# Optimization experiments

Hardware: AMD Instinct MI355X
Metric: run time of the kernel (lower is better)

## Reference

```python
import jax, jax.numpy as jnp
import numpy as np

N_NODES = 50000
N_EDGES = 800000
NFEAT = 96
NHID = 128
EPS = 1e-12  # F.normalize default eps


def setup_inputs() -> dict:
    key = jax.random.key(0)
    k1, k2, k3, k4 = jax.random.split(key, 4)
    edge_index = jax.random.randint(k1, (2, N_EDGES), 0, N_NODES, dtype=jnp.int64)
    x = jax.random.normal(k2, (N_NODES, NFEAT), dtype=jnp.float32)
    # Glorot-ish scaling for linear weights
    W_l = jax.random.normal(k3, (NHID, NFEAT), dtype=jnp.float32) * (1.0 / np.sqrt(NFEAT))
    b_l = jnp.zeros((NHID,), dtype=jnp.float32)
    W_r = jax.random.normal(k4, (NHID, NFEAT), dtype=jnp.float32) * (1.0 / np.sqrt(NFEAT))
    return {"edge_index": edge_index, "x": x, "W_l": W_l, "b_l": b_l, "W_r": W_r}


def reference(edge_index, x, W_l, b_l, W_r):
    # PyG SAGEConv, aggr='mean', root_weight=True, normalize=True
    src, dst = edge_index[0], edge_index[1]
    # gather source features, scatter-sum into destination nodes
    msg_sum = jax.ops.segment_sum(x[src], dst, num_segments=N_NODES)  # [N, nfeat]
    deg = jax.ops.segment_sum(jnp.ones((edge_index.shape[1],), dtype=x.dtype),
                              dst, num_segments=N_NODES)
    agg = msg_sum / jnp.maximum(deg, 1.0)[:, None]  # mean; isolated nodes -> 0
    out = agg @ W_l.T + b_l + x @ W_r.T  # [N, nhid]
    # L2 normalize per node (F.normalize p=2, dim=-1)
    norm = jnp.linalg.norm(out, axis=-1, keepdims=True)
    return out / jnp.maximum(norm, EPS)
```

## Files before the change

### kernel.cpp

```cpp
#include <hip/hip_runtime.h>


typedef __attribute__((ext_vector_type(8))) short short8;
typedef __attribute__((ext_vector_type(4))) float floatx4;

constexpr int kNodes = 50000;
constexpr int kEdges = 800000;
constexpr int kF = 96;
constexpr int kH = 128;
constexpr int kEllW = 32;
constexpr int kSpillCap = 4096;
constexpr int kBktRange = kNodes / 8;

constexpr size_t kXhOff    = 0;
constexpr size_t kWhOff    = 19200000;
constexpr size_t kEllOff   = 19249152;
constexpr size_t kCurOff   = 22449152;
constexpr size_t kSpcOff   = 22649152;
constexpr size_t kSpillOff = 22649168;

constexpr int kPeriods    = 782;
constexpr int kMegaBlocks = kPeriods * 11;
constexpr int kPrepBlocks = kPeriods * 3;
constexpr int kPrepItems  = kNodes * kF / 8 + kH * 192 / 8;
constexpr int kPrepStride = kPrepBlocks * 256;

constexpr int kRowS = 104;

__device__ __forceinline__ unsigned pack2_bf16(float a, float b) {
  unsigned ua = __float_as_uint(a), ub = __float_as_uint(b);
  ua = (ua + 0x7fffu + ((ua >> 16) & 1u)) >> 16;
  ub = (ub + 0x7fffu + ((ub >> 16) & 1u)) >> 16;
  return ua | (ub << 16);
}
__device__ __forceinline__ float bf_lo(unsigned u) { return __uint_as_float(u << 16); }
__device__ __forceinline__ float bf_hi(unsigned u) { return __uint_as_float(u & 0xffff0000u); }

__device__ __forceinline__ void ell_insert(int dst, int src, int* cursor,
                                           ushort* ell, unsigned* spill,
                                           int* spillCnt) {
  const int slot = atomicAdd(&cursor[dst], 1);
  if (slot < kEllW) {
    ell[(size_t)dst * kEllW + ((slot & 3) << 3) + (slot >> 2)] = (ushort)src;
  } else {
    const int sp = atomicAdd(spillCnt, 1);
    if (sp < kSpillCap) spill[sp] = ((unsigned)dst << 16) | (unsigned)src;
  }
}

__global__ void __launch_bounds__(256)
mega_kernel(const int* __restrict__ ei, const float* __restrict__ x,
            const float* __restrict__ Wl, const float* __restrict__ Wr,
            uint4* __restrict__ xh4, uint4* __restrict__ wh4,
            int* __restrict__ cursor, ushort* __restrict__ ell,
            unsigned* __restrict__ spill, int* __restrict__ spillCnt) {
  const int p = blockIdx.x / 11;
  const int r = blockIdx.x % 11;
  if (r < 8) {
    const int g = blockIdx.x & 7;
    const int lo = g * kBktRange, hi = lo + kBktRange;
    const int base = p * 1024 + threadIdx.x;
    int d[4];
#pragma unroll
    for (int k = 0; k < 4; ++k) {
      const int e = base + k * 256;
      d[k] = (e < kEdges) ? ei[kEdges + e] : -1;
    }
#pragma unroll
    for (int k = 0; k < 4; ++k) {
      if (d[k] >= lo && d[k] < hi) {
        const int e = base + k * 256;
        ell_insert(d[k], ei[e], cursor, ell, spill, spillCnt);
      }
    }
    return;
  }
  constexpr int kCvt = kNodes * kF / 8;
  const int pid = p * 3 + (r - 8);
  for (int i = pid * 256 + threadIdx.x; i < kPrepItems; i += kPrepStride) {
    if (i < kCvt) {
      const float4 v0 = reinterpret_cast<const float4*>(x)[i * 2];
      const float4 v1 = reinterpret_cast<const float4*>(x)[i * 2 + 1];
      uint4 o;
      o.x = pack2_bf16(v0.x, v0.y);
      o.y = pack2_bf16(v0.z, v0.w);
      o.z = pack2_bf16(v1.x, v1.y);
      o.w = pack2_bf16(v1.z, v1.w);
      xh4[i] = o;
    } else {
      const int j = i - kCvt;
      const int row = j / 24, chunk = j % 24;
      const float* src = (chunk < 12) ? (Wl + (size_t)row * kF + chunk * 8)
                                      : (Wr + (size_t)row * kF + (chunk - 12) * 8);
      const float4 v0 = reinterpret_cast<const float4*>(src)[0];
      const float4 v1 = reinterpret_cast<const float4*>(src)[1];
      uint4 o;
      o.x = pack2_bf16(v0.x, v0.y);
      o.y = pack2_bf16(v0.z, v0.w);
      o.z = pack2_bf16(v1.x, v1.y);
      o.w = pack2_bf16(v1.z, v1.w);
      wh4[j] = o;
    }
  }
}

__global__ void __launch_bounds__(256)
gm_kernel(const uint4* __restrict__ xh4, const int* __restrict__ cursor,
          const ushort* __restrict__ ell, const unsigned* __restrict__ spill,
          const int* __restrict__ spillCnt, const uint4* __restrict__ wh4,
          const float* __restrict__ bl, float* __restrict__ out) {
  __shared__ __align__(16) short sAgg[16 * kRowS];
  __shared__ float sP[4][4][4];

  const int wave = threadIdx.x >> 6, lane = threadIdx.x & 63;
  const int g = blockIdx.x & 7;
  const int j = blockIdx.x >> 3;
  const int tstart = (g * 3125) >> 3;
  const int tend = ((g + 1) * 3125) >> 3;
  const int tile = tstart + j;
  if (tile >= tend) return;
  const int base = tile * 16;

  const int slot = lane / 12;
  const int c = lane % 12;
  const bool gactive = lane < 48;
  const int slotc = gactive ? slot : 0;
  const int sc = min(*spillCnt, kSpillCap);

#pragma unroll
  for (int it = 0; it < 2; ++it) {
    const int nA = base + wave * 4 + it * 2;
    const int nB = nA + 1;
    const int degA = cursor[nA];
    const int degB = cursor[nB];
    const int dmA = min(degA, kEllW);
    const int dmB = min(degB, kEllW);

    const uint4 ivA = *reinterpret_cast<const uint4*>(
        ell + (size_t)nA * kEllW + (slotc << 3));
    const uint4 ivB = *reinterpret_cast<const uint4*>(
        ell + (size_t)nB * kEllW + (slotc << 3));
    const unsigned wa[4] = {ivA.x, ivA.y, ivA.z, ivA.w};
    const unsigned wb[4] = {ivB.x, ivB.y, ivB.z, ivB.w};

    float a0 = 0.f, a1 = 0.f, a2 = 0.f, a3 = 0.f,
          a4 = 0.f, a5 = 0.f, a6 = 0.f, a7 = 0.f;
    float b0 = 0.f, b1 = 0.f, b2 = 0.f, b3 = 0.f,
          b4 = 0.f, b5 = 0.f, b6 = 0.f, b7 = 0.f;

#pragma unroll
    for (int k = 0; k < 8; ++k) {
      const int idx = (k << 2) + slot;
      const int srcA = (k & 1) ? (int)(wa[k >> 1] >> 16) : (int)(wa[k >> 1] & 0xffffu);
      const int srcB = (k & 1) ? (int)(wb[k >> 1] >> 16) : (int)(wb[k >> 1] & 0xffffu);
      if (gactive && idx < dmA) {
        const uint4 v = xh4[(size_t)srcA * 12 + c];
        a0 += bf_lo(v.x); a1 += bf_hi(v.x);
        a2 += bf_lo(v.y); a3 += bf_hi(v.y);
        a4 += bf_lo(v.z); a5 += bf_hi(v.z);
        a6 += bf_lo(v.w); a7 += bf_hi(v.w);
      }
      if (gactive && idx < dmB) {
        const uint4 v = xh4[(size_t)srcB * 12 + c];
        b0 += bf_lo(v.x); b1 += bf_hi(v.x);
        b2 += bf_lo(v.y); b3 += bf_hi(v.y);
        b4 += bf_lo(v.z); b5 += bf_hi(v.z);
        b6 += bf_lo(v.w); b7 += bf_hi(v.w);
      }
    }
    for (int jj = 0; jj < sc; ++jj) {
      const unsigned pr = spill[jj];
      const int pd = (int)(pr >> 16);
      if (lane < 12 && (pd == nA || pd == nB)) {
        const uint4 v = xh4[(size_t)(pr & 0xffffu) * 12 + c];
        if (pd == nA) {
          a0 += bf_lo(v.x); a1 += bf_hi(v.x);
          a2 += bf_lo(v.y); a3 += bf_hi(v.y);
          a4 += bf_lo(v.z); a5 += bf_hi(v.z);
          a6 += bf_lo(v.w); a7 += bf_hi(v.w);
        } else {
          b0 += bf_lo(v.x); b1 += bf_hi(v.x);
          b2 += bf_lo(v.y); b3 += bf_hi(v.y);
          b4 += bf_lo(v.z); b5 += bf_hi(v.z);
          b6 += bf_lo(v.w); b7 += bf_hi(v.w);
        }
      }
    }
    a0 += __shfl(a0, lane + 24, 64); a1 += __shfl(a1, lane + 24, 64);
    a2 += __shfl(a2, lane + 24, 64); a3 += __shfl(a3, lane + 24, 64);
    a4 += __shfl(a4, lane + 24, 64); a5 += __shfl(a5, lane + 24, 64);
    a6 += __shfl(a6, lane + 24, 64); a7 += __shfl(a7, lane + 24, 64);
    a0 += __shfl(a0, lane + 12, 64); a1 += __shfl(a1, lane + 12, 64);
    a2 += __shfl(a2, lane + 12, 64); a3 += __shfl(a3, lane + 12, 64);
    a4 += __shfl(a4, lane + 12, 64); a5 += __shfl(a5, lane + 12, 64);
    a6 += __shfl(a6, lane + 12, 64); a7 += __shfl(a7, lane + 12, 64);
    b0 += __shfl(b0, lane + 24, 64); b1 += __shfl(b1, lane + 24, 64);
    b2 += __shfl(b2, lane + 24, 64); b3 += __shfl(b3, lane + 24, 64);
    b4 += __shfl(b4, lane + 24, 64); b5 += __shfl(b5, lane + 24, 64);
    b6 += __shfl(b6, lane + 24, 64); b7 += __shfl(b7, lane + 24, 64);
    b0 += __shfl(b0, lane + 12, 64); b1 += __shfl(b1, lane + 12, 64);
    b2 += __shfl(b2, lane + 12, 64); b3 += __shfl(b3, lane + 12, 64);
    b4 += __shfl(b4, lane + 12, 64); b5 += __shfl(b5, lane + 12, 64);
    b6 += __shfl(b6, lane + 12, 64); b7 += __shfl(b7, lane + 12, 64);

    if (lane < 12) {
      const float invA = 1.0f / fmaxf((float)degA, 1.0f);
      uint4 o;
      o.x = pack2_bf16(a0 * invA, a1 * invA);
      o.y = pack2_bf16(a2 * invA, a3 * invA);
      o.z = pack2_bf16(a4 * invA, a5 * invA);
      o.w = pack2_bf16(a6 * invA, a7 * invA);
      *reinterpret_cast<uint4*>(&sAgg[(wave * 4 + it * 2) * kRowS + c * 8]) = o;
      const float invB = 1.0f / fmaxf((float)degB, 1.0f);
      uint4 p;
      p.x = pack2_bf16(b0 * invB, b1 * invB);
      p.y = pack2_bf16(b2 * invB, b3 * invB);
      p.z = pack2_bf16(b4 * invB, b5 * invB);
      p.w = pack2_bf16(b6 * invB, b7 * invB);
      *reinterpret_cast<uint4*>(&sAgg[(wave * 4 + it * 2 + 1) * kRowS + c * 8]) = p;
    }
  }
  __syncthreads();

  const int r = lane & 15, q = lane >> 4;
  const int cg0 = wave * 2;
  const short8* xhS = reinterpret_cast<const short8*>(xh4);
  const short8* whS = reinterpret_cast<const short8*>(wh4);

  floatx4 acc[2] = {};
#pragma unroll
  for (int ks = 0; ks < 6; ++ks) {
    short8 a;
    if (ks < 3) {
      a = *reinterpret_cast<const short8*>(&sAgg[r * kRowS + (ks * 4 + q) * 8]);
    } else {
      a = xhS[(size_t)(base + r) * 12 + (ks - 3) * 4 + q];
    }
#pragma unroll
    for (int i = 0; i < 2; ++i) {
      const short8 b = whS[((cg0 + i) * 16 + r) * 24 + ks * 4 + q];
      acc[i] = __builtin_amdgcn_mfma_f32_16x16x32_bf16(a, b, acc[i], 0, 0, 0);
    }
  }

  float p0 = 0.f, p1 = 0.f, p2 = 0.f, p3 = 0.f;
#pragma unroll
  for (int i = 0; i < 2; ++i) {
    const float bb = bl[(cg0 + i) * 16 + r];
    acc[i][0] += bb; acc[i][1] += bb; acc[i][2] += bb; acc[i][3] += bb;
    p0 += acc[i][0] * acc[i][0];
    p1 += acc[i][1] * acc[i][1];
    p2 += acc[i][2] * acc[i][2];
    p3 += acc[i][3] * acc[i][3];
  }
#pragma unroll
  for (int off = 1; off < 16; off <<= 1) {
    p0 += __shfl_xor(p0, off, 64);
    p1 += __shfl_xor(p1, off, 64);
    p2 += __shfl_xor(p2, off, 64);
    p3 += __shfl_xor(p3, off, 64);
  }
  if (r == 0) {
    sP[wave][q][0] = p0; sP[wave][q][1] = p1;
    sP[wave][q][2] = p2; sP[wave][q][3] = p3;
  }
  __syncthreads();
  const float t0 = sP[0][q][0] + sP[1][q][0] + sP[2][q][0] + sP[3][q][0];
  const float t1 = sP[0][q][1] + sP[1][q][1] + sP[2][q][1] + sP[3][q][1];
  const float t2 = sP[0][q][2] + sP[1][q][2] + sP[2][q][2] + sP[3][q][2];
  const float t3 = sP[0][q][3] + sP[1][q][3] + sP[2][q][3] + sP[3][q][3];
  const float s0 = 1.0f / fmaxf(sqrtf(t0), 1e-12f);
  const float s1 = 1.0f / fmaxf(sqrtf(t1), 1e-12f);
  const float s2 = 1.0f / fmaxf(sqrtf(t2), 1e-12f);
  const float s3 = 1.0f / fmaxf(sqrtf(t3), 1e-12f);

#pragma unroll
  for (int i = 0; i < 2; ++i) {
    const int col = (cg0 + i) * 16 + r;
    float* o = out + (size_t)(base + q * 4) * kH + col;
    o[0 * kH] = acc[i][0] * s0;
    o[1 * kH] = acc[i][1] * s1;
    o[2 * kH] = acc[i][2] * s2;
    o[3 * kH] = acc[i][3] * s3;
  }
}

extern "C" void kernel_launch(void* const* d_in, const int* in_sizes, int n_in,
                              void* d_out, int out_size, void* d_ws, size_t ws_size,
                              hipStream_t stream) {
  const int*   ei = (const int*)d_in[0];
  const float* x  = (const float*)d_in[1];
  const float* Wl = (const float*)d_in[2];
  const float* bl = (const float*)d_in[3];
  const float* Wr = (const float*)d_in[4];
  float* out = (float*)d_out;

  char* ws = (char*)d_ws;
  uint4*    xh4      = (uint4*)(ws + kXhOff);
  uint4*    wh4      = (uint4*)(ws + kWhOff);
  ushort*   ell      = (ushort*)(ws + kEllOff);
  int*      cursor   = (int*)(ws + kCurOff);
  int*      spillCnt = (int*)(ws + kSpcOff);
  unsigned* spill    = (unsigned*)(ws + kSpillOff);

  hipMemsetAsync(ws + kCurOff, 0, 200008, stream);

  mega_kernel<<<kMegaBlocks, 256, 0, stream>>>(ei, x, Wl, Wr, xh4, wh4, cursor,
                                               ell, spill, spillCnt);

  gm_kernel<<<391 * 8, 256, 0, stream>>>(xh4, cursor, ell, spill, spillCnt,
                                         wh4, bl, out);
}
```

Baseline: 101.0 us.

## Pad degree counters to cache-line stride and gather four nodes per pass

Degree/cursor counters are spread to one per 64-byte line to reduce atomic contention among neighbouring destination nodes during ELL construction. The aggregation step now loads ELL indices and degrees for four nodes up front and interleaves their gathers in a single loop, increasing outstanding memory requests. In exchange, the counter memset grows sixteenfold, degree reads become strided, and register pressure rises.

```diff
diff --git a/kernel.cpp b/kernel.cpp
--- a/kernel.cpp
+++ b/kernel.cpp
@@ -11,13 +11,14 @@
 constexpr int kEllW = 32;
 constexpr int kSpillCap = 4096;
 constexpr int kBktRange = kNodes / 8;
+constexpr int kCurStride = 16;
 
 constexpr size_t kXhOff    = 0;
 constexpr size_t kWhOff    = 19200000;
 constexpr size_t kEllOff   = 19249152;
 constexpr size_t kCurOff   = 22449152;
-constexpr size_t kSpcOff   = 22649152;
-constexpr size_t kSpillOff = 22649168;
+constexpr size_t kSpcOff   = 25649152;
+constexpr size_t kSpillOff = 25649168;
 
 constexpr int kPeriods    = 782;
 constexpr int kMegaBlocks = kPeriods * 11;
@@ -39,7 +40,7 @@
 __device__ __forceinline__ void ell_insert(int dst, int src, int* cursor,
                                            ushort* ell, unsigned* spill,
                                            int* spillCnt) {
-  const int slot = atomicAdd(&cursor[dst], 1);
+  const int slot = atomicAdd(&cursor[(size_t)dst * kCurStride], 1);
   if (slot < kEllW) {
     ell[(size_t)dst * kEllW + ((slot & 3) << 3) + (slot >> 2)] = (ushort)src;
   } else {
@@ -126,98 +127,77 @@
   const bool gactive = lane < 48;
   const int slotc = gactive ? slot : 0;
   const int sc = min(*spillCnt, kSpillCap);
-
-#pragma unroll
-  for (int it = 0; it < 2; ++it) {
-    const int nA = base + wave * 4 + it * 2;
-    const int nB = nA + 1;
-    const int degA = cursor[nA];
-    const int degB = cursor[nB];
-    const int dmA = min(degA, kEllW);
-    const int dmB = min(degB, kEllW);
-
-    const uint4 ivA = *reinterpret_cast<const uint4*>(
-        ell + (size_t)nA * kEllW + (slotc << 3));
-    const uint4 ivB = *reinterpret_cast<const uint4*>(
-        ell + (size_t)nB * kEllW + (slotc << 3));
-    const unsigned wa[4] = {ivA.x, ivA.y, ivA.z, ivA.w};
-    const unsigned wb[4] = {ivB.x, ivB.y, ivB.z, ivB.w};
-
-    float a0 = 0.f, a1 = 0.f, a2 = 0.f, a3 = 0.f,
-          a4 = 0.f, a5 = 0.f, a6 = 0.f, a7 = 0.f;
-    float b0 = 0.f, b1 = 0.f, b2 = 0.f, b3 = 0.f,
-          b4 = 0.f, b5 = 0.f, b6 = 0.f, b7 = 0.f;
-
-#pragma unroll
-    for (int k = 0; k < 8; ++k) {
-      const int idx = (k << 2) + slot;
-      const int srcA = (k & 1) ? (int)(wa[k >> 1] >> 16) : (int)(wa[k >> 1] & 0xffffu);
-      const int srcB = (k & 1) ? (int)(wb[k >> 1] >> 16) : (int)(wb[k >> 1] & 0xffffu);
-      if (gactive && idx < dmA) {
-        const uint4 v = xh4[(size_t)srcA * 12 + c];
-        a0 += bf_lo(v.x); a1 += bf_hi(v.x);
-        a2 += bf_lo(v.y); a3 += bf_hi(v.y);
-        a4 += bf_lo(v.z); a5 += bf_hi(v.z);
-        a6 += bf_lo(v.w); a7 += bf_hi(v.w);
+  const int n0 = base + wave * 4;
+
+  int deg[4], dm[4];
+  uint4 iv[4];
+#pragma unroll
+  for (int n = 0; n < 4; ++n) {
+    deg[n] = cursor[(size_t)(n0 + n) * kCurStride];
+    iv[n] = *reinterpret_cast<const uint4*>(
+        ell + (size_t)(n0 + n) * kEllW + (slotc << 3));
+  }
+#pragma unroll
+  for (int n = 0; n < 4; ++n) dm[n] = min(deg[n], kEllW);
+
+  float acc[4][8];
+#pragma unroll
+  for (int n = 0; n < 4; ++n)
+#pragma unroll
+    for (int k = 0; k < 8; ++k) acc[n][k] = 0.f;
+
+#pragma unroll
+  for (int k = 0; k < 8; ++k) {
+    const int idx = (k << 2) + slot;
+#pragma unroll
+    for (int n = 0; n < 4; ++n) {
+      const unsigned wrd = (k < 2) ? iv[n].x
+                         : (k < 4) ? iv[n].y
+                         : (k < 6) ? iv[n].z : iv[n].w;
+      const int src = (k & 1) ? (int)(wrd >> 16) : (int)(wrd & 0xffffu);
+      if (gactive && idx < dm[n]) {
+        const uint4 v = xh4[(size_t)src * 12 + c];
+        acc[n][0] += bf_lo(v.x); acc[n][1] += bf_hi(v.x);
+        acc[n][2] += bf_lo(v.y); acc[n][3] += bf_hi(v.y);
+        acc[n][4] += bf_lo(v.z); acc[n][5] += bf_hi(v.z);
+        acc[n][6] += bf_lo(v.w); acc[n][7] += bf_hi(v.w);
       }
-      if (gactive && idx < dmB) {
-        const uint4 v = xh4[(size_t)srcB * 12 + c];
-        b0 += bf_lo(v.x); b1 += bf_hi(v.x);
-        b2 += bf_lo(v.y); b3 += bf_hi(v.y);
-        b4 += bf_lo(v.z); b5 += bf_hi(v.z);
-        b6 += bf_lo(v.w); b7 += bf_hi(v.w);
-      }
-    }
-    for (int jj = 0; jj < sc; ++jj) {
-      const unsigned pr = spill[jj];
-      const int pd = (int)(pr >> 16);
-      if (lane < 12 && (pd == nA || pd == nB)) {
-        const uint4 v = xh4[(size_t)(pr & 0xffffu) * 12 + c];
-        if (pd == nA) {
-          a0 += bf_lo(v.x); a1 += bf_hi(v.x);
-          a2 += bf_lo(v.y); a3 += bf_hi(v.y);
-          a4 += bf_lo(v.z); a5 += bf_hi(v.z);
-          a6 += bf_lo(v.w); a7 += bf_hi(v.w);
-        } else {
-          b0 += bf_lo(v.x); b1 += bf_hi(v.x);
-          b2 += bf_lo(v.y); b3 += bf_hi(v.y);
-          b4 += bf_lo(v.z); b5 += bf_hi(v.z);
-          b6 += bf_lo(v.w); b7 += bf_hi(v.w);
+    }
+  }
+  for (int jj = 0; jj < sc; ++jj) {
+    const unsigned pr = spill[jj];
+    const int rel = (int)(pr >> 16) - n0;
+    if (lane < 12 && rel >= 0 && rel < 4) {
+      const uint4 v = xh4[(size_t)(pr & 0xffffu) * 12 + c];
+#pragma unroll
+      for (int n = 0; n < 4; ++n) {
+        if (rel == n) {
+          acc[n][0] += bf_lo(v.x); acc[n][1] += bf_hi(v.x);
+          acc[n][2] += bf_lo(v.y); acc[n][3] += bf_hi(v.y);
+          acc[n][4] += bf_lo(v.z); acc[n][5] += bf_hi(v.z);
+          acc[n][6] += bf_lo(v.w); acc[n][7] += bf_hi(v.w);
         }
       }
     }
-    a0 += __shfl(a0, lane + 24, 64); a1 += __shfl(a1, lane + 24, 64);
-    a2 += __shfl(a2, lane + 24, 64); a3 += __shfl(a3, lane + 24, 64);
-    a4 += __shfl(a4, lane + 24, 64); a5 += __shfl(a5, lane + 24, 64);
-    a6 += __shfl(a6, lane + 24, 64); a7 += __shfl(a7, lane + 24, 64);
-    a0 += __shfl(a0, lane + 12, 64); a1 += __shfl(a1, lane + 12, 64);
-    a2 += __shfl(a2, lane + 12, 64); a3 += __shfl(a3, lane + 12, 64);
-    a4 += __shfl(a4, lane + 12, 64); a5 += __shfl(a5, lane + 12, 64);
-    a6 += __shfl(a6, lane + 12, 64); a7 += __shfl(a7, lane + 12, 64);
-    b0 += __shfl(b0, lane + 24, 64); b1 += __shfl(b1, lane + 24, 64);
-    b2 += __shfl(b2, lane + 24, 64); b3 += __shfl(b3, lane + 24, 64);
-    b4 += __shfl(b4, lane + 24, 64); b5 += __shfl(b5, lane + 24, 64);
-    b6 += __shfl(b6, lane + 24, 64); b7 += __shfl(b7, lane + 24, 64);
-    b0 += __shfl(b0, lane + 12, 64); b1 += __shfl(b1, lane + 12, 64);
-    b2 += __shfl(b2, lane + 12, 64); b3 += __shfl(b3, lane + 12, 64);
-    b4 += __shfl(b4, lane + 12, 64); b5 += __shfl(b5, lane + 12, 64);
-    b6 += __shfl(b6, lane + 12, 64); b7 += __shfl(b7, lane + 12, 64);
-
-    if (lane < 12) {
-      const float invA = 1.0f / fmaxf((float)degA, 1.0f);
+  }
+#pragma unroll
+  for (int n = 0; n < 4; ++n) {
+#pragma unroll
+    for (int k = 0; k < 8; ++k) {
+      acc[n][k] += __shfl(acc[n][k], lane + 24, 64);
+      acc[n][k] += __shfl(acc[n][k], lane + 12, 64);
+    }
+  }
+  if (lane < 12) {
+#pragma unroll
+    for (int n = 0; n < 4; ++n) {
+      const float inv = 1.0f / fmaxf((float)deg[n], 1.0f);
       uint4 o;
-      o.x = pack2_bf16(a0 * invA, a1 * invA);
-      o.y = pack2_bf16(a2 * invA, a3 * invA);
-      o.z = pack2_bf16(a4 * invA, a5 * invA);
-      o.w = pack2_bf16(a6 * invA, a7 * invA);
-      *reinterpret_cast<uint4*>(&sAgg[(wave * 4 + it * 2) * kRowS + c * 8]) = o;
-      const float invB = 1.0f / fmaxf((float)degB, 1.0f);
-      uint4 p;
-      p.x = pack2_bf16(b0 * invB, b1 * invB);
-      p.y = pack2_bf16(b2 * invB, b3 * invB);
-      p.z = pack2_bf16(b4 * invB, b5 * invB);
-      p.w = pack2_bf16(b6 * invB, b7 * invB);
-      *reinterpret_cast<uint4*>(&sAgg[(wave * 4 + it * 2 + 1) * kRowS + c * 8]) = p;
+      o.x = pack2_bf16(acc[n][0] * inv, acc[n][1] * inv);
+      o.y = pack2_bf16(acc[n][2] * inv, acc[n][3] * inv);
+      o.z = pack2_bf16(acc[n][4] * inv, acc[n][5] * inv);
+      o.w = pack2_bf16(acc[n][6] * inv, acc[n][7] * inv);
+      *reinterpret_cast<uint4*>(&sAgg[(wave * 4 + n) * kRowS + c * 8]) = o;
     }
   }
   __syncthreads();
@@ -227,7 +207,7 @@
   const short8* xhS = reinterpret_cast<const short8*>(xh4);
   const short8* whS = reinterpret_cast<const short8*>(wh4);
 
-  floatx4 acc[2] = {};
+  floatx4 fac[2] = {};
 #pragma unroll
   for (int ks = 0; ks < 6; ++ks) {
     short8 a;
@@ -239,7 +219,7 @@
 #pragma unroll
     for (int i = 0; i < 2; ++i) {
       const short8 b = whS[((cg0 + i) * 16 + r) * 24 + ks * 4 + q];
-      acc[i] = __builtin_amdgcn_mfma_f32_16x16x32_bf16(a, b, acc[i], 0, 0, 0);
+      fac[i] = __builtin_amdgcn_mfma_f32_16x16x32_bf16(a, b, fac[i], 0, 0, 0);
     }
   }
 
@@ -247,11 +227,11 @@
 #pragma unroll
   for (int i = 0; i < 2; ++i) {
     const float bb = bl[(cg0 + i) * 16 + r];
-    acc[i][0] += bb; acc[i][1] += bb; acc[i][2] += bb; acc[i][3] += bb;
-    p0 += acc[i][0] * acc[i][0];
-    p1 += acc[i][1] * acc[i][1];
-    p2 += acc[i][2] * acc[i][2];
-    p3 += acc[i][3] * acc[i][3];
+    fac[i][0] += bb; fac[i][1] += bb; fac[i][2] += bb; fac[i][3] += bb;
+    p0 += fac[i][0] * fac[i][0];
+    p1 += fac[i][1] * fac[i][1];
+    p2 += fac[i][2] * fac[i][2];
+    p3 += fac[i][3] * fac[i][3];
   }
 #pragma unroll
   for (int off = 1; off < 16; off <<= 1) {
@@ -278,10 +258,10 @@
   for (int i = 0; i < 2; ++i) {
     const int col = (cg0 + i) * 16 + r;
     float* o = out + (size_t)(base + q * 4) * kH + col;
-    o[0 * kH] = acc[i][0] * s0;
-    o[1 * kH] = acc[i][1] * s1;
-    o[2 * kH] = acc[i][2] * s2;
-    o[3 * kH] = acc[i][3] * s3;
+    o[0 * kH] = fac[i][0] * s0;
+    o[1 * kH] = fac[i][1] * s1;
+    o[2 * kH] = fac[i][2] * s2;
+    o[3 * kH] = fac[i][3] * s3;
   }
 }
 
@@ -303,7 +283,7 @@
   int*      spillCnt = (int*)(ws + kSpcOff);
   unsigned* spill    = (unsigned*)(ws + kSpillOff);
 
-  hipMemsetAsync(ws + kCurOff, 0, 200008, stream);
+  hipMemsetAsync(ws + kCurOff, 0, 3200008, stream);
 
   mega_kernel<<<kMegaBlocks, 256, 0, stream>>>(ei, x, Wl, Wr, xh4, wh4, cursor,
                                                ell, spill, spillCnt);
```

Measured after the change: 102.4 us. About the same (+1.3%).

## Pad degree cursors to 64B stride and use 8 waves per gather tile

Applied to the files above, without the earlier changes.

Each node's degree counter now sits on its own 64-byte slot, so atomics from different nodes no longer contend on the same cache line. The memset grows from 200 KB to 3.2 MB to clear the padded array. The aggregate-and-project kernel now runs 512 threads per block: each wave gathers neighbours for two nodes instead of four and issues one MFMA output column group instead of two. This adds gather parallelism, but the extra memset traffic and the scattered degree reads are new costs.

```diff
diff --git a/kernel.cpp b/kernel.cpp
--- a/kernel.cpp
+++ b/kernel.cpp
@@ -11,13 +11,14 @@
 constexpr int kEllW = 32;
 constexpr int kSpillCap = 4096;
 constexpr int kBktRange = kNodes / 8;
+constexpr int kCurStride = 16;
 
 constexpr size_t kXhOff    = 0;
 constexpr size_t kWhOff    = 19200000;
 constexpr size_t kEllOff   = 19249152;
 constexpr size_t kCurOff   = 22449152;
-constexpr size_t kSpcOff   = 22649152;
-constexpr size_t kSpillOff = 22649168;
+constexpr size_t kSpcOff   = 25649152;
+constexpr size_t kSpillOff = 25649168;
 
 constexpr int kPeriods    = 782;
 constexpr int kMegaBlocks = kPeriods * 11;
@@ -39,7 +40,7 @@
 __device__ __forceinline__ void ell_insert(int dst, int src, int* cursor,
                                            ushort* ell, unsigned* spill,
                                            int* spillCnt) {
-  const int slot = atomicAdd(&cursor[dst], 1);
+  const int slot = atomicAdd(&cursor[(size_t)dst * kCurStride], 1);
   if (slot < kEllW) {
     ell[(size_t)dst * kEllW + ((slot & 3) << 3) + (slot >> 2)] = (ushort)src;
   } else {
@@ -104,13 +105,13 @@
   }
 }
 
-__global__ void __launch_bounds__(256)
+__global__ void __launch_bounds__(512)
 gm_kernel(const uint4* __restrict__ xh4, const int* __restrict__ cursor,
           const ushort* __restrict__ ell, const unsigned* __restrict__ spill,
           const int* __restrict__ spillCnt, const uint4* __restrict__ wh4,
           const float* __restrict__ bl, float* __restrict__ out) {
   __shared__ __align__(16) short sAgg[16 * kRowS];
-  __shared__ float sP[4][4][4];
+  __shared__ float sP[8][4][4];
 
   const int wave = threadIdx.x >> 6, lane = threadIdx.x & 63;
   const int g = blockIdx.x & 7;
@@ -127,107 +128,104 @@
   const int slotc = gactive ? slot : 0;
   const int sc = min(*spillCnt, kSpillCap);
 
-#pragma unroll
-  for (int it = 0; it < 2; ++it) {
-    const int nA = base + wave * 4 + it * 2;
-    const int nB = nA + 1;
-    const int degA = cursor[nA];
-    const int degB = cursor[nB];
-    const int dmA = min(degA, kEllW);
-    const int dmB = min(degB, kEllW);
-
-    const uint4 ivA = *reinterpret_cast<const uint4*>(
-        ell + (size_t)nA * kEllW + (slotc << 3));
-    const uint4 ivB = *reinterpret_cast<const uint4*>(
-        ell + (size_t)nB * kEllW + (slotc << 3));
-    const unsigned wa[4] = {ivA.x, ivA.y, ivA.z, ivA.w};
-    const unsigned wb[4] = {ivB.x, ivB.y, ivB.z, ivB.w};
-
-    float a0 = 0.f, a1 = 0.f, a2 = 0.f, a3 = 0.f,
-          a4 = 0.f, a5 = 0.f, a6 = 0.f, a7 = 0.f;
-    float b0 = 0.f, b1 = 0.f, b2 = 0.f, b3 = 0.f,
-          b4 = 0.f, b5 = 0.f, b6 = 0.f, b7 = 0.f;
-
-#pragma unroll
-    for (int k = 0; k < 8; ++k) {
-      const int idx = (k << 2) + slot;
-      const int srcA = (k & 1) ? (int)(wa[k >> 1] >> 16) : (int)(wa[k >> 1] & 0xffffu);
-      const int srcB = (k & 1) ? (int)(wb[k >> 1] >> 16) : (int)(wb[k >> 1] & 0xffffu);
-      if (gactive && idx < dmA) {
-        const uint4 v = xh4[(size_t)srcA * 12 + c];
+  const int nA = base + wave * 2;
+  const int nB = nA + 1;
+  const int degA = cursor[(size_t)nA * kCurStride];
+  const int degB = cursor[(size_t)nB * kCurStride];
+  const int dmA = min(degA, kEllW);
+  const int dmB = min(degB, kEllW);
+
+  const uint4 ivA = *reinterpret_cast<const uint4*>(
+      ell + (size_t)nA * kEllW + (slotc << 3));
+  const uint4 ivB = *reinterpret_cast<const uint4*>(
+      ell + (size_t)nB * kEllW + (slotc << 3));
+  const unsigned wa[4] = {ivA.x, ivA.y, ivA.z, ivA.w};
+  const unsigned wb[4] = {ivB.x, ivB.y, ivB.z, ivB.w};
+
+  float a0 = 0.f, a1 = 0.f, a2 = 0.f, a3 = 0.f,
+        a4 = 0.f, a5 = 0.f, a6 = 0.f, a7 = 0.f;
+  float b0 = 0.f, b1 = 0.f, b2 = 0.f, b3 = 0.f,
+        b4 = 0.f, b5 = 0.f, b6 = 0.f, b7 = 0.f;
+
+#pragma unroll
+  for (int k = 0; k < 8; ++k) {
+    const int idx = (k << 2) + slot;
+    const int srcA = (k & 1) ? (int)(wa[k >> 1] >> 16) : (int)(wa[k >> 1] & 0xffffu);
+    const int srcB = (k & 1) ? (int)(wb[k >> 1] >> 16) : (int)(wb[k >> 1] & 0xffffu);
+    if (gactive && idx < dmA) {
+      const uint4 v = xh4[(size_t)srcA * 12 + c];
+      a0 += bf_lo(v.x); a1 += bf_hi(v.x);
+      a2 += bf_lo(v.y); a3 += bf_hi(v.y);
+      a4 += bf_lo(v.z); a5 += bf_hi(v.z);
+      a6 += bf_lo(v.w); a7 += bf_hi(v.w);
+    }
+    if (gactive && idx < dmB) {
+      const uint4 v = xh4[(size_t)srcB * 12 + c];
+      b0 += bf_lo(v.x); b1 += bf_hi(v.x);
+      b2 += bf_lo(v.y); b3 += bf_hi(v.y);
+      b4 += bf_lo(v.z); b5 += bf_hi(v.z);
+      b6 += bf_lo(v.w); b7 += bf_hi(v.w);
+    }
+  }
+  for (int jj = 0; jj < sc; ++jj) {
+    const unsigned pr = spill[jj];
+    const int pd = (int)(pr >> 16);
+    if (lane < 12 && (pd == nA || pd == nB)) {
+      const uint4 v = xh4[(size_t)(pr & 0xffffu) * 12 + c];
+      if (pd == nA) {
         a0 += bf_lo(v.x); a1 += bf_hi(v.x);
         a2 += bf_lo(v.y); a3 += bf_hi(v.y);
         a4 += bf_lo(v.z); a5 += bf_hi(v.z);
         a6 += bf_lo(v.w); a7 += bf_hi(v.w);
-      }
-      if (gactive && idx < dmB) {
-        const uint4 v = xh4[(size_t)srcB * 12 + c];
+      } else {
         b0 += bf_lo(v.x); b1 += bf_hi(v.x);
         b2 += bf_lo(v.y); b3 += bf_hi(v.y);
         b4 += bf_lo(v.z); b5 += bf_hi(v.z);
         b6 += bf_lo(v.w); b7 += bf_hi(v.w);
       }
     }
-    for (int jj = 0; jj < sc; ++jj) {
-      const unsigned pr = spill[jj];
-      const int pd = (int)(pr >> 16);
-      if (lane < 12 && (pd == nA || pd == nB)) {
-        const uint4 v = xh4[(size_t)(pr & 0xffffu) * 12 + c];
-        if (pd == nA) {
-          a0 += bf_lo(v.x); a1 += bf_hi(v.x);
-          a2 += bf_lo(v.y); a3 += bf_hi(v.y);
-          a4 += bf_lo(v.z); a5 += bf_hi(v.z);
-          a6 += bf_lo(v.w); a7 += bf_hi(v.w);
-        } else {
-          b0 += bf_lo(v.x); b1 += bf_hi(v.x);
-          b2 += bf_lo(v.y); b3 += bf_hi(v.y);
-          b4 += bf_lo(v.z); b5 += bf_hi(v.z);
-          b6 += bf_lo(v.w); b7 += bf_hi(v.w);
-        }
-      }
-    }
-    a0 += __shfl(a0, lane + 24, 64); a1 += __shfl(a1, lane + 24, 64);
-    a2 += __shfl(a2, lane + 24, 64); a3 += __shfl(a3, lane + 24, 64);
-    a4 += __shfl(a4, lane + 24, 64); a5 += __shfl(a5, lane + 24, 64);
-    a6 += __shfl(a6, lane + 24, 64); a7 += __shfl(a7, lane + 24, 64);
-    a0 += __shfl(a0, lane + 12, 64); a1 += __shfl(a1, lane + 12, 64);
-    a2 += __shfl(a2, lane + 12, 64); a3 += __shfl(a3, lane + 12, 64);
-    a4 += __shfl(a4, lane + 12, 64); a5 += __shfl(a5, lane + 12, 64);
-    a6 += __shfl(a6, lane + 12, 64); a7 += __shfl(a7, lane + 12, 64);
-    b0 += __shfl(b0, lane + 24, 64); b1 += __shfl(b1, lane + 24, 64);
-    b2 += __shfl(b2, lane + 24, 64); b3 += __shfl(b3, lane + 24, 64);
-    b4 += __shfl(b4, lane + 24, 64); b5 += __shfl(b5, lane + 24, 64);
-    b6 += __shfl(b6, lane + 24, 64); b7 += __shfl(b7, lane + 24, 64);
-    b0 += __shfl(b0, lane + 12, 64); b1 += __shfl(b1, lane + 12, 64);
-    b2 += __shfl(b2, lane + 12, 64); b3 += __shfl(b3, lane + 12, 64);
-    b4 += __shfl(b4, lane + 12, 64); b5 += __shfl(b5, lane + 12, 64);
-    b6 += __shfl(b6, lane + 12, 64); b7 += __shfl(b7, lane + 12, 64);
-
-    if (lane < 12) {
-      const float invA = 1.0f / fmaxf((float)degA, 1.0f);
-      uint4 o;
-      o.x = pack2_bf16(a0 * invA, a1 * invA);
-      o.y = pack2_bf16(a2 * invA, a3 * invA);
-      o.z = pack2_bf16(a4 * invA, a5 * invA);
-      o.w = pack2_bf16(a6 * invA, a7 * invA);
-      *reinterpret_cast<uint4*>(&sAgg[(wave * 4 + it * 2) * kRowS + c * 8]) = o;
-      const float invB = 1.0f / fmaxf((float)degB, 1.0f);
-      uint4 p;
-      p.x = pack2_bf16(b0 * invB, b1 * invB);
-      p.y = pack2_bf16(b2 * invB, b3 * invB);
-      p.z = pack2_bf16(b4 * invB, b5 * invB);
-      p.w = pack2_bf16(b6 * invB, b7 * invB);
-      *reinterpret_cast<uint4*>(&sAgg[(wave * 4 + it * 2 + 1) * kRowS + c * 8]) = p;
-    }
+  }
+  a0 += __shfl(a0, lane + 24, 64); a1 += __shfl(a1, lane + 24, 64);
+  a2 += __shfl(a2, lane + 24, 64); a3 += __shfl(a3, lane + 24, 64);
+  a4 += __shfl(a4, lane + 24, 64); a5 += __shfl(a5, lane + 24, 64);
+  a6 += __shfl(a6, lane + 24, 64); a7 += __shfl(a7, lane + 24, 64);
+  a0 += __shfl(a0, lane + 12, 64); a1 += __shfl(a1, lane + 12, 64);
+  a2 += __shfl(a2, lane + 12, 64); a3 += __shfl(a3, lane + 12, 64);
+  a4 += __shfl(a4, lane + 12, 64); a5 += __shfl(a5, lane + 12, 64);
+  a6 += __shfl(a6, lane + 12, 64); a7 += __shfl(a7, lane + 12, 64);
+  b0 += __shfl(b0, lane + 24, 64); b1 += __shfl(b1, lane + 24, 64);
+  b2 += __shfl(b2, lane + 24, 64); b3 += __shfl(b3, lane + 24, 64);
+  b4 += __shfl(b4, lane + 24, 64); b5 += __shfl(b5, lane + 24, 64);
+  b6 += __shfl(b6, lane + 24, 64); b7 += __shfl(b7, lane + 24, 64);
+  b0 += __shfl(b0, lane + 12, 64); b1 += __shfl(b1, lane + 12, 64);
+  b2 += __shfl(b2, lane + 12, 64); b3 += __shfl(b3, lane + 12, 64);
+  b4 += __shfl(b4, lane + 12, 64); b5 += __shfl(b5, lane + 12, 64);
+  b6 += __shfl(b6, lane + 12, 64); b7 += __shfl(b7, lane + 12, 64);
+
+  if (lane < 12) {
+    const float invA = 1.0f / fmaxf((float)degA, 1.0f);
+    uint4 o;
+    o.x = pack2_bf16(a0 * invA, a1 * invA);
+    o.y = pack2_bf16(a2 * invA, a3 * invA);
+    o.z = pack2_bf16(a4 * invA, a5 * invA);
+    o.w = pack2_bf16(a6 * invA, a7 * invA);
+    *reinterpret_cast<uint4*>(&sAgg[(wave * 2) * kRowS + c * 8]) = o;
+    const float invB = 1.0f / fmaxf((float)degB, 1.0f);
+    uint4 p;
+    p.x = pack2_bf16(b0 * invB, b1 * invB);
+    p.y = pack2_bf16(b2 * invB, b3 * invB);
+    p.z = pack2_bf16(b4 * invB, b5 * invB);
+    p.w = pack2_bf16(b6 * invB, b7 * invB);
+    *reinterpret_cast<uint4*>(&sAgg[(wave * 2 + 1) * kRowS + c * 8]) = p;
   }
   __syncthreads();
 
   const int r = lane & 15, q = lane >> 4;
-  const int cg0 = wave * 2;
+  const int cg = wave;
   const short8* xhS = reinterpret_cast<const short8*>(xh4);
   const short8* whS = reinterpret_cast<const short8*>(wh4);
 
-  floatx4 acc[2] = {};
+  floatx4 fac = {};
 #pragma unroll
   for (int ks = 0; ks < 6; ++ks) {
     short8 a;
@@ -236,23 +234,16 @@
     } else {
       a = xhS[(size_t)(base + r) * 12 + (ks - 3) * 4 + q];
     }
-#pragma unroll
-    for (int i = 0; i < 2; ++i) {
-      const short8 b = whS[((cg0 + i) * 16 + r) * 24 + ks * 4 + q];
-      acc[i] = __builtin_amdgcn_mfma_f32_16x16x32_bf16(a, b, acc[i], 0, 0, 0);
-    }
-  }
-
-  float p0 = 0.f, p1 = 0.f, p2 = 0.f, p3 = 0.f;
-#pragma unroll
-  for (int i = 0; i < 2; ++i) {
-    const float bb = bl[(cg0 + i) * 16 + r];
-    acc[i][0] += bb; acc[i][1] += bb; acc[i][2] += bb; acc[i][3] += bb;
-    p0 += acc[i][0] * acc[i][0];
-    p1 += acc[i][1] * acc[i][1];
-    p2 += acc[i][2] * acc[i][2];
-    p3 += acc[i][3] * acc[i][3];
-  }
+    const short8 b = whS[(cg * 16 + r) * 24 + ks * 4 + q];
+    fac = __builtin_amdgcn_mfma_f32_16x16x32_bf16(a, b, fac, 0, 0, 0);
+  }
+
+  const float bb = bl[cg * 16 + r];
+  fac[0] += bb; fac[1] += bb; fac[2] += bb; fac[3] += bb;
+  float p0 = fac[0] * fac[0];
+  float p1 = fac[1] * fac[1];
+  float p2 = fac[2] * fac[2];
+  float p3 = fac[3] * fac[3];
 #pragma unroll
   for (int off = 1; off < 16; off <<= 1) {
     p0 += __shfl_xor(p0, off, 64);
@@ -265,24 +256,23 @@
     sP[wave][q][2] = p2; sP[wave][q][3] = p3;
   }
   __syncthreads();
-  const float t0 = sP[0][q][0] + sP[1][q][0] + sP[2][q][0] + sP[3][q][0];
-  const float t1 = sP[0][q][1] + sP[1][q][1] + sP[2][q][1] + sP[3][q][1];
-  const float t2 = sP[0][q][2] + sP[1][q][2] + sP[2][q][2] + sP[3][q][2];
-  const float t3 = sP[0][q][3] + sP[1][q][3] + sP[2][q][3] + sP[3][q][3];
+  float t0 = 0.f, t1 = 0.f, t2 = 0.f, t3 = 0.f;
+#pragma unroll
+  for (int w = 0; w < 8; ++w) {
+    t0 += sP[w][q][0]; t1 += sP[w][q][1];
+    t2 += sP[w][q][2]; t3 += sP[w][q][3];
+  }
   const float s0 = 1.0f / fmaxf(sqrtf(t0), 1e-12f);
   const float s1 = 1.0f / fmaxf(sqrtf(t1), 1e-12f);
   const float s2 = 1.0f / fmaxf(sqrtf(t2), 1e-12f);
   const float s3 = 1.0f / fmaxf(sqrtf(t3), 1e-12f);
 
-#pragma unroll
-  for (int i = 0; i < 2; ++i) {
-    const int col = (cg0 + i) * 16 + r;
-    float* o = out + (size_t)(base + q * 4) * kH + col;
-    o[0 * kH] = acc[i][0] * s0;
-    o[1 * kH] = acc[i][1] * s1;
-    o[2 * kH] = acc[i][2] * s2;
-    o[3 * kH] = acc[i][3] * s3;
-  }
+  const int col = cg * 16 + r;
+  float* o = out + (size_t)(base + q * 4) * kH + col;
+  o[0 * kH] = fac[0] * s0;
+  o[1 * kH] = fac[1] * s1;
+  o[2 * kH] = fac[2] * s2;
+  o[3 * kH] = fac[3] * s3;
 }
 
 extern "C" void kernel_launch(void* const* d_in, const int* in_sizes, int n_in,
@@ -303,11 +293,11 @@
   int*      spillCnt = (int*)(ws + kSpcOff);
   unsigned* spill    = (unsigned*)(ws + kSpillOff);
 
-  hipMemsetAsync(ws + kCurOff, 0, 200008, stream);
+  hipMemsetAsync(ws + kCurOff, 0, 3200008, stream);
 
   mega_kernel<<<kMegaBlocks, 256, 0, stream>>>(ei, x, Wl, Wr, xh4, wh4, cursor,
                                                ell, spill, spillCnt);
 
-  gm_kernel<<<391 * 8, 256, 0, stream>>>(xh4, cursor, ell, spill, spillCnt,
+  gm_kernel<<<391 * 8, 512, 0, stream>>>(xh4, cursor, ell, spill, spillCnt,
                                          wh4, bl, out);
 }
```

Measured after the change: 103.4 us. 1.02x slower.

## Stage edges into per-chunk destination buckets and pad cursor atomics to separate lines

Applied to the files above, without the earlier changes.

Edge scattering becomes two passes. The first pass reads each edge once and bins it into per-chunk, per-bucket staging lists in global memory, using LDS counters for the bin positions. A new fill kernel then performs the ELL inserts bucket by bucket, so earlier blocks no longer each re-read all edges and discard 7/8 of them. Cursor counters are padded to a 16-int stride so that atomics on neighbouring nodes land on different cache lines. In exchange there is an extra kernel launch, extra global staging traffic, and a memset that grows from about 200 KB to about 3.2 MB.

```diff
diff --git a/kernel.cpp b/kernel.cpp
--- a/kernel.cpp
+++ b/kernel.cpp
@@ -11,19 +11,23 @@
 constexpr int kEllW = 32;
 constexpr int kSpillCap = 4096;
 constexpr int kBktRange = kNodes / 8;
+constexpr int kCurStride = 16;
+constexpr int kChunksP = 782;
+constexpr int kStgCap = 256;
 
 constexpr size_t kXhOff    = 0;
+constexpr size_t kStgOff   = 9600000;
 constexpr size_t kWhOff    = 19200000;
 constexpr size_t kEllOff   = 19249152;
 constexpr size_t kCurOff   = 22449152;
-constexpr size_t kSpcOff   = 22649152;
-constexpr size_t kSpillOff = 22649168;
-
-constexpr int kPeriods    = 782;
-constexpr int kMegaBlocks = kPeriods * 11;
-constexpr int kPrepBlocks = kPeriods * 3;
-constexpr int kPrepItems  = kNodes * kF / 8 + kH * 192 / 8;
-constexpr int kPrepStride = kPrepBlocks * 256;
+constexpr size_t kSpcOff   = 25649152;
+constexpr size_t kSpillOff = 25649168;
+constexpr size_t kCntOff   = 25665552;
+
+constexpr int kMega2Blocks = kChunksP * 4;
+constexpr int kPrepBlocks  = kChunksP * 3;
+constexpr int kPrepItems   = kNodes * kF / 8 + kH * 192 / 8;
+constexpr int kPrepStride  = kPrepBlocks * 256;
 
 constexpr int kRowS = 104;
 
@@ -39,7 +43,7 @@
 __device__ __forceinline__ void ell_insert(int dst, int src, int* cursor,
                                            ushort* ell, unsigned* spill,
                                            int* spillCnt) {
-  const int slot = atomicAdd(&cursor[dst], 1);
+  const int slot = atomicAdd(&cursor[(size_t)dst * kCurStride], 1);
   if (slot < kEllW) {
     ell[(size_t)dst * kEllW + ((slot & 3) << 3) + (slot >> 2)] = (ushort)src;
   } else {
@@ -49,34 +53,46 @@
 }
 
 __global__ void __launch_bounds__(256)
-mega_kernel(const int* __restrict__ ei, const float* __restrict__ x,
-            const float* __restrict__ Wl, const float* __restrict__ Wr,
-            uint4* __restrict__ xh4, uint4* __restrict__ wh4,
-            int* __restrict__ cursor, ushort* __restrict__ ell,
-            unsigned* __restrict__ spill, int* __restrict__ spillCnt) {
-  const int p = blockIdx.x / 11;
-  const int r = blockIdx.x % 11;
-  if (r < 8) {
-    const int g = blockIdx.x & 7;
-    const int lo = g * kBktRange, hi = lo + kBktRange;
+mega2_kernel(const int* __restrict__ ei, const float* __restrict__ x,
+             const float* __restrict__ Wl, const float* __restrict__ Wr,
+             uint4* __restrict__ xh4, uint4* __restrict__ wh4,
+             unsigned* __restrict__ stg, int* __restrict__ cnt,
+             int* __restrict__ cursor, ushort* __restrict__ ell,
+             unsigned* __restrict__ spill, int* __restrict__ spillCnt) {
+  const int p = blockIdx.x >> 2;
+  const int r = blockIdx.x & 3;
+  if (r == 0) {
+    __shared__ int lcnt[8];
+    if (threadIdx.x < 8) lcnt[threadIdx.x] = 0;
+    __syncthreads();
     const int base = p * 1024 + threadIdx.x;
-    int d[4];
+    int d[4], s[4];
 #pragma unroll
     for (int k = 0; k < 4; ++k) {
       const int e = base + k * 256;
-      d[k] = (e < kEdges) ? ei[kEdges + e] : -1;
+      const bool v = e < kEdges;
+      d[k] = v ? ei[kEdges + e] : -1;
+      s[k] = v ? ei[e] : 0;
     }
 #pragma unroll
     for (int k = 0; k < 4; ++k) {
-      if (d[k] >= lo && d[k] < hi) {
-        const int e = base + k * 256;
-        ell_insert(d[k], ei[e], cursor, ell, spill, spillCnt);
+      if (d[k] >= 0) {
+        const int b = d[k] / kBktRange;
+        const int pos = atomicAdd(&lcnt[b], 1);
+        if (pos < kStgCap)
+          stg[((size_t)p * 8 + b) * kStgCap + pos] =
+              ((unsigned)d[k] << 16) | (unsigned)s[k];
+        else
+          ell_insert(d[k], s[k], cursor, ell, spill, spillCnt);
       }
     }
+    __syncthreads();
+    if (threadIdx.x < 8)
+      cnt[p * 8 + threadIdx.x] = min(lcnt[threadIdx.x], kStgCap);
     return;
   }
   constexpr int kCvt = kNodes * kF / 8;
-  const int pid = p * 3 + (r - 8);
+  const int pid = p * 3 + (r - 1);
   for (int i = pid * 256 + threadIdx.x; i < kPrepItems; i += kPrepStride) {
     if (i < kCvt) {
       const float4 v0 = reinterpret_cast<const float4*>(x)[i * 2];
@@ -105,6 +121,22 @@
 }
 
 __global__ void __launch_bounds__(256)
+fillp_kernel(const unsigned* __restrict__ stg, const int* __restrict__ cnt,
+             int* __restrict__ cursor, ushort* __restrict__ ell,
+             unsigned* __restrict__ spill, int* __restrict__ spillCnt) {
+  const int g = blockIdx.x & 7;
+  for (int chunk = blockIdx.x >> 3; chunk < kChunksP; chunk += gridDim.x >> 3) {
+    const int n = cnt[chunk * 8 + g];
+    const unsigned* reg = stg + ((size_t)chunk * 8 + g) * kStgCap;
+    for (int i = threadIdx.x; i < n; i += 256) {
+      const unsigned pr = reg[i];
+      ell_insert((int)(pr >> 16), (int)(pr & 0xffffu), cursor, ell, spill,
+                 spillCnt);
+    }
+  }
+}
+
+__global__ void __launch_bounds__(256)
 gm_kernel(const uint4* __restrict__ xh4, const int* __restrict__ cursor,
           const ushort* __restrict__ ell, const unsigned* __restrict__ spill,
           const int* __restrict__ spillCnt, const uint4* __restrict__ wh4,
@@ -131,8 +163,8 @@
   for (int it = 0; it < 2; ++it) {
     const int nA = base + wave * 4 + it * 2;
     const int nB = nA + 1;
-    const int degA = cursor[nA];
-    const int degB = cursor[nB];
+    const int degA = cursor[(size_t)nA * kCurStride];
+    const int degB = cursor[(size_t)nB * kCurStride];
     const int dmA = min(degA, kEllW);
     const int dmB = min(degB, kEllW);
 
@@ -227,7 +259,7 @@
   const short8* xhS = reinterpret_cast<const short8*>(xh4);
   const short8* whS = reinterpret_cast<const short8*>(wh4);
 
-  floatx4 acc[2] = {};
+  floatx4 fac[2] = {};
 #pragma unroll
   for (int ks = 0; ks < 6; ++ks) {
     short8 a;
@@ -239,7 +271,7 @@
 #pragma unroll
     for (int i = 0; i < 2; ++i) {
       const short8 b = whS[((cg0 + i) * 16 + r) * 24 + ks * 4 + q];
-      acc[i] = __builtin_amdgcn_mfma_f32_16x16x32_bf16(a, b, acc[i], 0, 0, 0);
+      fac[i] = __builtin_amdgcn_mfma_f32_16x16x32_bf16(a, b, fac[i], 0, 0, 0);
     }
   }
 
@@ -247,11 +279,11 @@
 #pragma unroll
   for (int i = 0; i < 2; ++i) {
     const float bb = bl[(cg0 + i) * 16 + r];
-    acc[i][0] += bb; acc[i][1] += bb; acc[i][2] += bb; acc[i][3] += bb;
-    p0 += acc[i][0] * acc[i][0];
-    p1 += acc[i][1] * acc[i][1];
-    p2 += acc[i][2] * acc[i][2];
-    p3 += acc[i][3] * acc[i][3];
+    fac[i][0] += bb; fac[i][1] += bb; fac[i][2] += bb; fac[i][3] += bb;
+    p0 += fac[i][0] * fac[i][0];
+    p1 += fac[i][1] * fac[i][1];
+    p2 += fac[i][2] * fac[i][2];
+    p3 += fac[i][3] * fac[i][3];
   }
 #pragma unroll
   for (int off = 1; off < 16; off <<= 1) {
@@ -278,10 +310,10 @@
   for (int i = 0; i < 2; ++i) {
     const int col = (cg0 + i) * 16 + r;
     float* o = out + (size_t)(base + q * 4) * kH + col;
-    o[0 * kH] = acc[i][0] * s0;
-    o[1 * kH] = acc[i][1] * s1;
-    o[2 * kH] = acc[i][2] * s2;
-    o[3 * kH] = acc[i][3] * s3;
+    o[0 * kH] = fac[i][0] * s0;
+    o[1 * kH] = fac[i][1] * s1;
+    o[2 * kH] = fac[i][2] * s2;
+    o[3 * kH] = fac[i][3] * s3;
   }
 }
 
@@ -297,16 +329,20 @@
 
   char* ws = (char*)d_ws;
   uint4*    xh4      = (uint4*)(ws + kXhOff);
+  unsigned* stg      = (unsigned*)(ws + kStgOff);
   uint4*    wh4      = (uint4*)(ws + kWhOff);
   ushort*   ell      = (ushort*)(ws + kEllOff);
   int*      cursor   = (int*)(ws + kCurOff);
   int*      spillCnt = (int*)(ws + kSpcOff);
   unsigned* spill    = (unsigned*)(ws + kSpillOff);
-
-  hipMemsetAsync(ws + kCurOff, 0, 200008, stream);
-
-  mega_kernel<<<kMegaBlocks, 256, 0, stream>>>(ei, x, Wl, Wr, xh4, wh4, cursor,
-                                               ell, spill, spillCnt);
+  int*      cnt      = (int*)(ws + kCntOff);
+
+  hipMemsetAsync(ws + kCurOff, 0, 3200032, stream);
+
+  mega2_kernel<<<kMega2Blocks, 256, 0, stream>>>(
+      ei, x, Wl, Wr, xh4, wh4, stg, cnt, cursor, ell, spill, spillCnt);
+
+  fillp_kernel<<<3128, 256, 0, stream>>>(stg, cnt, cursor, ell, spill, spillCnt);
 
   gm_kernel<<<391 * 8, 256, 0, stream>>>(xh4, cursor, ell, spill, spillCnt,
                                          wh4, bl, out);
```

Result: no change. 102.5 us (+1.4%).
